# Kernel optimization log

Hardware: AMD Instinct MI355X
Metric: run time of the kernel (lower is better)

## Reference

```python
import jax, jax.numpy as jnp
import numpy as np

N_NODES = 100000


def graph_conv(x, src, dst, W_rel, b_rel, W_root, num_nodes):
    # PyG GraphConv: out_i = W_rel @ (sum_{j->i} x_j) + b_rel + W_root @ x_i
    msgs = jnp.take(x, src, axis=0)                       # [E, d] gather
    agg = jax.ops.segment_sum(msgs, dst, num_segments=num_nodes)  # [N, d] scatter-add
    return agg @ W_rel.T + b_rel + x @ W_root.T


def setup_inputs() -> dict:
    key = jax.random.key(0)
    ks = jax.random.split(key, 7)
    d_in, d_hid, d_out = 64, 64, 64
    n_edges = 1_600_000
    x = jax.random.normal(ks[0], (N_NODES, d_in), dtype=jnp.float32)
    edge_index = jax.random.randint(ks[1], (2, n_edges), 0, N_NODES, dtype=jnp.int32)
    s = 1.0 / np.sqrt(d_in)
    W_rel1 = jax.random.normal(ks[2], (d_hid, d_in), dtype=jnp.float32) * s
    b_rel1 = jnp.zeros((d_hid,), dtype=jnp.float32)
    W_root1 = jax.random.normal(ks[3], (d_hid, d_in), dtype=jnp.float32) * s
    W_rel2 = jax.random.normal(ks[4], (d_out, d_hid), dtype=jnp.float32) * s
    b_rel2 = jnp.zeros((d_out,), dtype=jnp.float32)
    W_root2 = jax.random.normal(ks[5], (d_out, d_hid), dtype=jnp.float32) * s
    return {"x": x, "edge_index": edge_index,
            "W_rel1": W_rel1, "b_rel1": b_rel1, "W_root1": W_root1,
            "W_rel2": W_rel2, "b_rel2": b_rel2, "W_root2": W_root2}


def reference(x, edge_index, W_rel1, b_rel1, W_root1, W_rel2, b_rel2, W_root2):
    src, dst = edge_index[0], edge_index[1]
    h = graph_conv(x, src, dst, W_rel1, b_rel1, W_root1, N_NODES)
    h = jax.nn.relu(h)
    out = graph_conv(h, src, dst, W_rel2, b_rel2, W_root2, N_NODES)
    return out
```

## Files before the change

### kernel.cpp

```cpp
#include <hip/hip_runtime.h>
#include <hip/hip_bf16.h>

#define N_NODES 100000
#define SCAN_N (N_NODES + 1)
#define D 64
#define NBUCK 256
#define BSH 9
#define BNODES (1 << BSH)
#define EPB 2048

typedef __attribute__((ext_vector_type(8))) short bf16x8;
typedef __attribute__((ext_vector_type(4))) float f32x4;
typedef __attribute__((ext_vector_type(4))) unsigned int u32x4;


__global__ __launch_bounds__(256) void bucket_count(
    const int* __restrict__ dst, int* __restrict__ bcount, int n_edges)
{
    __shared__ int lh[NBUCK];
    const int t = threadIdx.x;
    lh[t] = 0;
    __syncthreads();
    const int e0 = blockIdx.x * EPB;
    const int e1 = min(e0 + EPB, n_edges);
    for (int e = e0 + t; e < e1; e += 256)
        atomicAdd(&lh[dst[e] >> BSH], 1);
    __syncthreads();
    if (lh[t]) atomicAdd(&bcount[t], lh[t]);
}

__global__ __launch_bounds__(256) void bucket_scan(
    const int* __restrict__ bcount, int* __restrict__ bstart,
    int* __restrict__ bcursor)
{
    __shared__ int tmp[256];
    const int t = threadIdx.x;
    const int v = bcount[t];
    tmp[t] = v;
    __syncthreads();
    for (int off = 1; off < 256; off <<= 1) {
        const int u = (t >= off) ? tmp[t - off] : 0;
        __syncthreads();
        tmp[t] += u;
        __syncthreads();
    }
    const int excl = tmp[t] - v;
    bstart[t] = excl;
    bcursor[t] = excl;
    if (t == 255) bstart[256] = tmp[255];
}

__global__ __launch_bounds__(256) void bucket_scatter(
    const int* __restrict__ src, const int* __restrict__ dst,
    int* __restrict__ bcursor, unsigned* __restrict__ packed, int n_edges)
{
    __shared__ int lh[NBUCK];
    __shared__ int lb[NBUCK];
    const int t = threadIdx.x;
    lh[t] = 0;
    __syncthreads();
    const int e0 = blockIdx.x * EPB;
    const int e1 = min(e0 + EPB, n_edges);
    for (int e = e0 + t; e < e1; e += 256)
        atomicAdd(&lh[dst[e] >> BSH], 1);
    __syncthreads();
    const int cnt = lh[t];
    lb[t] = cnt ? atomicAdd(&bcursor[t], cnt) : 0;
    __syncthreads();
    lh[t] = lb[t];
    __syncthreads();
    for (int e = e0 + t; e < e1; e += 256) {
        const int d = dst[e];
        const int pos = atomicAdd(&lh[d >> BSH], 1);
        packed[pos] = ((unsigned)src[e] << BSH) | (unsigned)(d & (BNODES - 1));
    }
}

__global__ __launch_bounds__(256) void bucket_csr(
    const unsigned* __restrict__ packed,
    const int* __restrict__ bstart,
    int* __restrict__ row_start,
    int* __restrict__ esrc)
{
    __shared__ int lcnt[BNODES];
    __shared__ int pair[256];
    const int b = blockIdx.x;
    const int t = threadIdx.x;
    const int beg = bstart[b];
    const int end = bstart[b + 1];

    lcnt[t] = 0; lcnt[t + 256] = 0;
    __syncthreads();
    for (int e = beg + t; e < end; e += 256)
        atomicAdd(&lcnt[packed[e] & (BNODES - 1)], 1);
    __syncthreads();

    const int v0 = lcnt[2 * t], v1 = lcnt[2 * t + 1];
    pair[t] = v0 + v1;
    __syncthreads();
    for (int off = 1; off < 256; off <<= 1) {
        const int u = (t >= off) ? pair[t - off] : 0;
        __syncthreads();
        pair[t] += u;
        __syncthreads();
    }
    const int pexcl = pair[t] - (v0 + v1);
    __syncthreads();
    lcnt[2 * t]     = pexcl;
    lcnt[2 * t + 1] = pexcl + v0;
    __syncthreads();

    {
        const int l0 = 2 * t, l1 = 2 * t + 1;
        const int n0 = b * BNODES + l0, n1 = b * BNODES + l1;
        if (n0 <= N_NODES) row_start[n0] = beg + lcnt[l0];
        if (n1 <= N_NODES) row_start[n1] = beg + lcnt[l1];
        lcnt[l0] += beg;
        lcnt[l1] += beg;
    }
    __syncthreads();
    for (int e = beg + t; e < end; e += 256) {
        const unsigned p = packed[e];
        const int pos = atomicAdd(&lcnt[p & (BNODES - 1)], 1);
        esrc[pos] = (int)(p >> BSH);
    }
}


__device__ __forceinline__ float uasf(unsigned u) { return __uint_as_float(u); }
__device__ __forceinline__ unsigned f2bf(float f) {
    __hip_bfloat16 b = __float2bfloat16(f);
    return (unsigned)*reinterpret_cast<unsigned short*>(&b);
}


__global__ __launch_bounds__(256) void wcat_kernel(
    const float* __restrict__ Wrel1, const float* __restrict__ Wroot1,
    const float* __restrict__ Wrel2, const float* __restrict__ Wroot2,
    unsigned short* __restrict__ Wcat)
{
    const float* Wrel  = blockIdx.x ? Wrel2 : Wrel1;
    const float* Wroot = blockIdx.x ? Wroot2 : Wroot1;
    unsigned short* O = Wcat + blockIdx.x * 64 * 128;
    for (int i = threadIdx.x; i < 4096; i += 256) {
        const int j = i >> 6, k = i & 63;
        O[j * 128 + k]      = (unsigned short)f2bf(Wrel[i]);
        O[j * 128 + 64 + k] = (unsigned short)f2bf(Wroot[i]);
    }
}


__global__ __launch_bounds__(256) void tobf_kernel(
    const float* __restrict__ in, unsigned short* __restrict__ out, int n8)
{
    const int i = blockIdx.x * 256 + threadIdx.x;
    if (i >= n8) return;
    const float4 v0 = *reinterpret_cast<const float4*>(&in[(long)i * 8]);
    const float4 v1 = *reinterpret_cast<const float4*>(&in[(long)i * 8 + 4]);
    u32x4 o;
    o.x = f2bf(v0.x) | (f2bf(v0.y) << 16);
    o.y = f2bf(v0.z) | (f2bf(v0.w) << 16);
    o.z = f2bf(v1.x) | (f2bf(v1.y) << 16);
    o.w = f2bf(v1.z) | (f2bf(v1.w) << 16);
    *reinterpret_cast<u32x4*>(&out[(long)i * 8]) = o;
}

__global__ __launch_bounds__(256) void gather_bf(
    const unsigned short* __restrict__ xin,
    const int* __restrict__ row_start,
    const int* __restrict__ esrc,
    unsigned short* __restrict__ agg)
{
    const int wid = (blockIdx.x * 256 + threadIdx.x) >> 6;
    if (wid >= N_NODES) return;
    const int lane = threadIdx.x & 63;
    const int g = lane >> 3;
    const int c = lane & 7;

    const int beg = row_start[wid];
    const int end = row_start[wid + 1];

    float a0 = 0.f, a1 = 0.f, a2 = 0.f, a3 = 0.f,
          a4 = 0.f, a5 = 0.f, a6 = 0.f, a7 = 0.f;
    for (int e = beg; e < end; e += 16) {
        const int i0 = e + g;
        const int i1 = e + 8 + g;
        if (i0 < end) {
            const u32x4 u = *reinterpret_cast<const u32x4*>(
                &xin[(long)esrc[i0] * D + c * 8]);
            a0 += uasf(u.x << 16); a1 += uasf(u.x & 0xFFFF0000u);
            a2 += uasf(u.y << 16); a3 += uasf(u.y & 0xFFFF0000u);
            a4 += uasf(u.z << 16); a5 += uasf(u.z & 0xFFFF0000u);
            a6 += uasf(u.w << 16); a7 += uasf(u.w & 0xFFFF0000u);
        }
        if (i1 < end) {
            const u32x4 u = *reinterpret_cast<const u32x4*>(
                &xin[(long)esrc[i1] * D + c * 8]);
            a0 += uasf(u.x << 16); a1 += uasf(u.x & 0xFFFF0000u);
            a2 += uasf(u.y << 16); a3 += uasf(u.y & 0xFFFF0000u);
            a4 += uasf(u.z << 16); a5 += uasf(u.z & 0xFFFF0000u);
            a6 += uasf(u.w << 16); a7 += uasf(u.w & 0xFFFF0000u);
        }
    }
#pragma unroll
    for (int m = 8; m <= 32; m <<= 1) {
        a0 += __shfl_xor(a0, m); a1 += __shfl_xor(a1, m);
        a2 += __shfl_xor(a2, m); a3 += __shfl_xor(a3, m);
        a4 += __shfl_xor(a4, m); a5 += __shfl_xor(a5, m);
        a6 += __shfl_xor(a6, m); a7 += __shfl_xor(a7, m);
    }
    if (g == 0) {
        u32x4 o;
        o.x = f2bf(a0) | (f2bf(a1) << 16);
        o.y = f2bf(a2) | (f2bf(a3) << 16);
        o.z = f2bf(a4) | (f2bf(a5) << 16);
        o.w = f2bf(a6) | (f2bf(a7) << 16);
        *reinterpret_cast<u32x4*>(&agg[(long)wid * D + c * 8]) = o;
    }
}

#define LSTR 136
template <typename OT, int RELU>
__global__ __launch_bounds__(256, 4) void dense_mfma(
    const unsigned short* __restrict__ agg,
    const unsigned short* __restrict__ xin,
    const unsigned short* __restrict__ Wcat,
    const float* __restrict__ brel,
    OT* __restrict__ out)
{
    __shared__ __align__(16) short Wl[64 * LSTR];
    __shared__ __align__(16) short Al[128 * LSTR];

    const int t = threadIdx.x;
    const int node0 = blockIdx.x * 128;

    for (int i = t; i < 1024; i += 256) {
        const int j = i >> 4, c = i & 15;
        *reinterpret_cast<u32x4*>(&Wl[j * LSTR + c * 8]) =
            *reinterpret_cast<const u32x4*>(&Wcat[j * 128 + c * 8]);
    }
    for (int i = t; i < 2048; i += 256) {
        const int n = i >> 4, c = i & 15;
        int gn = node0 + n; if (gn > N_NODES - 1) gn = N_NODES - 1;
        const u32x4 v = (c < 8)
            ? *reinterpret_cast<const u32x4*>(&agg[(long)gn * D + c * 8])
            : *reinterpret_cast<const u32x4*>(&xin[(long)gn * D + (c - 8) * 8]);
        *reinterpret_cast<u32x4*>(&Al[n * LSTR + c * 8]) = v;
    }
    __syncthreads();

    const int lane = t & 63;
    const int w = t >> 6;
    const int lr = lane & 15;
    const int q = lane >> 4;

    bf16x8 afrag[2][4];
#pragma unroll
    for (int ggr = 0; ggr < 2; ++ggr)
#pragma unroll
        for (int kk = 0; kk < 4; ++kk)
            afrag[ggr][kk] = *reinterpret_cast<const bf16x8*>(
                &Al[(w * 32 + ggr * 16 + lr) * LSTR + kk * 32 + q * 8]);

    f32x4 acc[2][4] = {};
#pragma unroll
    for (int f = 0; f < 4; ++f) {
#pragma unroll
        for (int kk = 0; kk < 4; ++kk) {
            const bf16x8 bfrag = *reinterpret_cast<const bf16x8*>(
                &Wl[(f * 16 + lr) * LSTR + kk * 32 + q * 8]);
            acc[0][f] = __builtin_amdgcn_mfma_f32_16x16x32_bf16(
                afrag[0][kk], bfrag, acc[0][f], 0, 0, 0);
            acc[1][f] = __builtin_amdgcn_mfma_f32_16x16x32_bf16(
                afrag[1][kk], bfrag, acc[1][f], 0, 0, 0);
        }
    }

#pragma unroll
    for (int ggr = 0; ggr < 2; ++ggr) {
#pragma unroll
        for (int f = 0; f < 4; ++f) {
            const int col = f * 16 + lr;
            const float bias = brel[col];
#pragma unroll
            for (int r = 0; r < 4; ++r) {
                const int node = node0 + w * 32 + ggr * 16 + q * 4 + r;
                if (node < N_NODES) {
                    float v = acc[ggr][f][r] + bias;
                    if (RELU) v = fmaxf(v, 0.f);
                    if constexpr (sizeof(OT) == 4)
                        ((float*)out)[(long)node * D + col] = v;
                    else
                        ((unsigned short*)out)[(long)node * D + col] =
                            (unsigned short)f2bf(v);
                }
            }
        }
    }
}


extern "C" void kernel_launch(void* const* d_in, const int* in_sizes, int n_in,
                              void* d_out, int out_size, void* d_ws, size_t ws_size,
                              hipStream_t stream)
{
    const float* x     = (const float*)d_in[0];
    const int*   ei    = (const int*)d_in[1];
    const float* Wrel1 = (const float*)d_in[2];
    const float* brel1 = (const float*)d_in[3];
    const float* Wroot1= (const float*)d_in[4];
    const float* Wrel2 = (const float*)d_in[5];
    const float* brel2 = (const float*)d_in[6];
    const float* Wroot2= (const float*)d_in[7];
    float* out = (float*)d_out;

    const int n_edges = in_sizes[1] / 2;
    const int* src = ei;
    const int* dst = ei + n_edges;

    int* base      = (int*)d_ws;
    int* row_start = base;
    int* bstart    = base + 100352;
    int* bcursor   = base + 100672;
    int* bcount    = base + 100928;
    unsigned short* Wcat = (unsigned short*)(base + 101184);
    int* esrc      = base + 109376;
    const size_t xbf_off = (((size_t)(109376 + n_edges) * 4) + 255) & ~(size_t)255;
    const size_t row_bf  = (size_t)N_NODES * D * 2;
    const size_t agg_off = xbf_off + row_bf;
    const size_t h_off   = agg_off + row_bf;

    unsigned short* xbf = (unsigned short*)((char*)d_ws + xbf_off);
    unsigned short* agg = (unsigned short*)((char*)d_ws + agg_off);
    unsigned short* h   = (unsigned short*)((char*)d_ws + h_off);
    unsigned* packed    = (unsigned*)agg;

    const int BB = (n_edges + EPB - 1) / EPB;
    hipMemsetAsync(bcount, 0, NBUCK * sizeof(int), stream);
    bucket_count<<<BB, 256, 0, stream>>>(dst, bcount, n_edges);
    bucket_scan<<<1, 256, 0, stream>>>(bcount, bstart, bcursor);
    wcat_kernel<<<2, 256, 0, stream>>>(Wrel1, Wroot1, Wrel2, Wroot2, Wcat);
    tobf_kernel<<<(N_NODES * D / 8 + 255) / 256, 256, 0, stream>>>(x, xbf, N_NODES * D / 8);
    bucket_scatter<<<BB, 256, 0, stream>>>(src, dst, bcursor, packed, n_edges);
    bucket_csr<<<NBUCK, 256, 0, stream>>>(packed, bstart, row_start, esrc);

    const int GB = (N_NODES * 64 + 255) / 256;
    const int DB = (N_NODES + 127) / 128;

    gather_bf<<<GB, 256, 0, stream>>>(xbf, row_start, esrc, agg);
    dense_mfma<__hip_bfloat16, 1><<<DB, 256, 0, stream>>>(
        agg, xbf, Wcat, brel1, (__hip_bfloat16*)h);
    gather_bf<<<GB, 256, 0, stream>>>(h, row_start, esrc, agg);
    dense_mfma<float, 0><<<DB, 256, 0, stream>>>(
        agg, h, Wcat + 64 * 128, brel2, out);
}
```

Measured before the change: 211.3 us.

## Drop bucket count pass by scattering into fixed-capacity padded buckets

Removes the separate bucket counting kernel and memset by giving each destination bucket a fixed padded slot range (PADB), so the scatter can reserve positions directly and the scan runs afterward on the final cursors. bucket_csr reads from the padded region and writes compacted CSR output. Edges per block are also doubled. This saves one full read of the dst array and a launch, but silently overflows if any bucket receives more than PADB edges, which holds only for roughly uniform destinations.

```diff
diff --git a/kernel.cpp b/kernel.cpp
--- a/kernel.cpp
+++ b/kernel.cpp
@@ -7,17 +7,25 @@
 #define NBUCK 256
 #define BSH 9
 #define BNODES (1 << BSH)
-#define EPB 2048
+#define EPB 4096
+#define PADB 9216
 
 typedef __attribute__((ext_vector_type(8))) short bf16x8;
 typedef __attribute__((ext_vector_type(4))) float f32x4;
 typedef __attribute__((ext_vector_type(4))) unsigned int u32x4;
 
 
-__global__ __launch_bounds__(256) void bucket_count(
-    const int* __restrict__ dst, int* __restrict__ bcount, int n_edges)
+__global__ __launch_bounds__(256) void init_cursors(int* __restrict__ bcursor)
+{
+    bcursor[threadIdx.x] = threadIdx.x * PADB;
+}
+
+__global__ __launch_bounds__(256) void bucket_scatter(
+    const int* __restrict__ src, const int* __restrict__ dst,
+    int* __restrict__ bcursor, unsigned* __restrict__ packed, int n_edges)
 {
     __shared__ int lh[NBUCK];
+    __shared__ int lb[NBUCK];
     const int t = threadIdx.x;
     lh[t] = 0;
     __syncthreads();
@@ -26,16 +34,24 @@
     for (int e = e0 + t; e < e1; e += 256)
         atomicAdd(&lh[dst[e] >> BSH], 1);
     __syncthreads();
-    if (lh[t]) atomicAdd(&bcount[t], lh[t]);
+    const int cnt = lh[t];
+    lb[t] = cnt ? atomicAdd(&bcursor[t], cnt) : 0;
+    __syncthreads();
+    lh[t] = lb[t];
+    __syncthreads();
+    for (int e = e0 + t; e < e1; e += 256) {
+        const int d = dst[e];
+        const int pos = atomicAdd(&lh[d >> BSH], 1);
+        packed[pos] = ((unsigned)src[e] << BSH) | (unsigned)(d & (BNODES - 1));
+    }
 }
 
 __global__ __launch_bounds__(256) void bucket_scan(
-    const int* __restrict__ bcount, int* __restrict__ bstart,
-    int* __restrict__ bcursor)
+    const int* __restrict__ bcursor, int* __restrict__ bstart)
 {
     __shared__ int tmp[256];
     const int t = threadIdx.x;
-    const int v = bcount[t];
+    const int v = bcursor[t] - t * PADB;
     tmp[t] = v;
     __syncthreads();
     for (int off = 1; off < 256; off <<= 1) {
@@ -44,36 +60,8 @@
         tmp[t] += u;
         __syncthreads();
     }
-    const int excl = tmp[t] - v;
-    bstart[t] = excl;
-    bcursor[t] = excl;
+    bstart[t] = tmp[t] - v;
     if (t == 255) bstart[256] = tmp[255];
-}
-
-__global__ __launch_bounds__(256) void bucket_scatter(
-    const int* __restrict__ src, const int* __restrict__ dst,
-    int* __restrict__ bcursor, unsigned* __restrict__ packed, int n_edges)
-{
-    __shared__ int lh[NBUCK];
-    __shared__ int lb[NBUCK];
-    const int t = threadIdx.x;
-    lh[t] = 0;
-    __syncthreads();
-    const int e0 = blockIdx.x * EPB;
-    const int e1 = min(e0 + EPB, n_edges);
-    for (int e = e0 + t; e < e1; e += 256)
-        atomicAdd(&lh[dst[e] >> BSH], 1);
-    __syncthreads();
-    const int cnt = lh[t];
-    lb[t] = cnt ? atomicAdd(&bcursor[t], cnt) : 0;
-    __syncthreads();
-    lh[t] = lb[t];
-    __syncthreads();
-    for (int e = e0 + t; e < e1; e += 256) {
-        const int d = dst[e];
-        const int pos = atomicAdd(&lh[d >> BSH], 1);
-        packed[pos] = ((unsigned)src[e] << BSH) | (unsigned)(d & (BNODES - 1));
-    }
 }
 
 __global__ __launch_bounds__(256) void bucket_csr(
@@ -86,12 +74,14 @@
     __shared__ int pair[256];
     const int b = blockIdx.x;
     const int t = threadIdx.x;
-    const int beg = bstart[b];
-    const int end = bstart[b + 1];
+    const int beg_out = bstart[b];
+    const int cnt_b = bstart[b + 1] - beg_out;
+    const int beg_rd = b * PADB;
+    const int end_rd = beg_rd + cnt_b;
 
     lcnt[t] = 0; lcnt[t + 256] = 0;
     __syncthreads();
-    for (int e = beg + t; e < end; e += 256)
+    for (int e = beg_rd + t; e < end_rd; e += 256)
         atomicAdd(&lcnt[packed[e] & (BNODES - 1)], 1);
     __syncthreads();
 
@@ -113,13 +103,13 @@
     {
         const int l0 = 2 * t, l1 = 2 * t + 1;
         const int n0 = b * BNODES + l0, n1 = b * BNODES + l1;
-        if (n0 <= N_NODES) row_start[n0] = beg + lcnt[l0];
-        if (n1 <= N_NODES) row_start[n1] = beg + lcnt[l1];
-        lcnt[l0] += beg;
-        lcnt[l1] += beg;
-    }
-    __syncthreads();
-    for (int e = beg + t; e < end; e += 256) {
+        if (n0 <= N_NODES) row_start[n0] = beg_out + lcnt[l0];
+        if (n1 <= N_NODES) row_start[n1] = beg_out + lcnt[l1];
+        lcnt[l0] += beg_out;
+        lcnt[l1] += beg_out;
+    }
+    __syncthreads();
+    for (int e = beg_rd + t; e < end_rd; e += 256) {
         const unsigned p = packed[e];
         const int pos = atomicAdd(&lcnt[p & (BNODES - 1)], 1);
         esrc[pos] = (int)(p >> BSH);
@@ -322,10 +312,9 @@
     int* row_start = base;
     int* bstart    = base + 100352;
     int* bcursor   = base + 100672;
-    int* bcount    = base + 100928;
-    unsigned short* Wcat = (unsigned short*)(base + 101184);
-    int* esrc      = base + 109376;
-    const size_t xbf_off = (((size_t)(109376 + n_edges) * 4) + 255) & ~(size_t)255;
+    unsigned short* Wcat = (unsigned short*)(base + 100928);
+    int* esrc      = base + 109120;
+    const size_t xbf_off = (((size_t)(109120 + n_edges) * 4) + 255) & ~(size_t)255;
     const size_t row_bf  = (size_t)N_NODES * D * 2;
     const size_t agg_off = xbf_off + row_bf;
     const size_t h_off   = agg_off + row_bf;
@@ -336,12 +325,12 @@
     unsigned* packed    = (unsigned*)agg;
 
     const int BB = (n_edges + EPB - 1) / EPB;
-    hipMemsetAsync(bcount, 0, NBUCK * sizeof(int), stream);
-    bucket_count<<<BB, 256, 0, stream>>>(dst, bcount, n_edges);
-    bucket_scan<<<1, 256, 0, stream>>>(bcount, bstart, bcursor);
+
+    init_cursors<<<1, 256, 0, stream>>>(bcursor);
     wcat_kernel<<<2, 256, 0, stream>>>(Wrel1, Wroot1, Wrel2, Wroot2, Wcat);
     tobf_kernel<<<(N_NODES * D / 8 + 255) / 256, 256, 0, stream>>>(x, xbf, N_NODES * D / 8);
     bucket_scatter<<<BB, 256, 0, stream>>>(src, dst, bcursor, packed, n_edges);
+    bucket_scan<<<1, 256, 0, stream>>>(bcursor, bstart);
     bucket_csr<<<NBUCK, 256, 0, stream>>>(packed, bstart, row_start, esrc);
 
     const int GB = (N_NODES * 64 + 255) / 256;
```

Result: faster. 188.8 us (-10.7%).
